# Kernel tuning notes

Hardware: AMD Instinct MI355X
Metric: run time of the kernel (lower is better)

Reference implementation:

```python
import jax, jax.numpy as jnp
import numpy as np


def setup_inputs() -> dict:
    key = jax.random.key(0)
    ks = jax.random.split(key, 8)
    B = 65536
    x = jax.random.normal(ks[0], (B, 784), dtype=jnp.float32)
    conv_w = jnp.ones((3, 3), dtype=jnp.float32)  # Parameter(ones((3,3)))
    # Linear layers stored as (in, out) weight + (out,) bias
    def lin(k, fin, fout):
        kw, kb = jax.random.split(k)
        bound = 1.0 / np.sqrt(fin)
        W = jax.random.uniform(kw, (fin, fout), minval=-bound, maxval=bound, dtype=jnp.float32)
        b = jax.random.uniform(kb, (fout,), minval=-bound, maxval=bound, dtype=jnp.float32)
        return W, b
    W1, b1 = lin(ks[1], 26 * 26, 500)
    W2, b2 = lin(ks[2], 500, 200)
    W3, b3 = lin(ks[3], 200, 10)
    return {"x": x, "conv_w": conv_w, "W1": W1, "b1": b1,
            "W2": W2, "b2": b2, "W3": W3, "b3": b3}


def reference(x, conv_w, W1, b1, W2, b2, W3, b3):
    B = x.shape[0]
    img = x.reshape(B, 1, 28, 28)  # NCHW, single channel
    kern = conv_w.reshape(1, 1, 3, 3)  # OIHW
    # valid 2D cross-correlation == torch tensordot sliding-window loop
    conv = jax.lax.conv_general_dilated(
        img, kern, window_strides=(1, 1), padding='VALID',
        dimension_numbers=('NCHW', 'OIHW', 'NCHW'))  # (B,1,26,26)
    h = conv.reshape(B, 26 * 26)
    h = jax.nn.relu(h @ W1 + b1)
    h = jax.nn.relu(h @ W2 + b2)
    return h @ W3 + b3  # (B, 10) logits
```

## Files before the change

### kernel.cpp

```cpp
#include <hip/hip_runtime.h>
#include <hip/hip_bf16.h>
#include <stdint.h>

typedef __bf16 bf16x8 __attribute__((ext_vector_type(8)));
typedef float  f32x4  __attribute__((ext_vector_type(4)));


#define KT1 25
#define NF1 32
#define KT2 16
#define NF2 16
#define KT3 8

__global__ void prep_w1(const float* __restrict__ W1, const float* __restrict__ cw,
                        __bf16* __restrict__ w1s) {
  int gid  = blockIdx.x * 256 + threadIdx.x;
  int lane = gid & 63;
  int slot = gid >> 6;
  int t = slot >> 5;
  int f = slot & 31;
  int kbase = t * 32 + ((lane >> 4) << 3);
  int n = f * 16 + (lane & 15);
  float c[9];
#pragma unroll
  for (int i = 0; i < 9; ++i) c[i] = cw[i];
  bf16x8 v;
#pragma unroll
  for (int e = 0; e < 8; ++e) {
    int k = kbase + e;
    float acc = 0.f;
    if (k < 784 && n < 500) {
      int pi = k / 28, pj = k % 28;
#pragma unroll
      for (int dr = 0; dr < 3; ++dr) {
        int r = pi - dr;
        if (r < 0 || r >= 26) continue;
#pragma unroll
        for (int dc = 0; dc < 3; ++dc) {
          int cc = pj - dc;
          if (cc < 0 || cc >= 26) continue;
          acc += c[dr * 3 + dc] * W1[(size_t)(r * 26 + cc) * 500 + n];
        }
      }
    }
    v[e] = (__bf16)acc;
  }
  *(bf16x8*)(w1s + (size_t)(slot * 64 + lane) * 8) = v;
}

__global__ void prep_w2(const float* __restrict__ W2, __bf16* __restrict__ w2s) {
  int gid  = blockIdx.x * 256 + threadIdx.x;
  int lane = gid & 63;
  int slot = gid >> 6;
  int t = slot >> 4;
  int f = slot & 15;
  int kbase = t * 32 + ((lane >> 4) << 3);
  int n = f * 16 + (lane & 15);
  bf16x8 v;
#pragma unroll
  for (int e = 0; e < 8; ++e) {
    int k = kbase + e;
    float val = (k < 500 && n < 200) ? W2[(size_t)k * 200 + n] : 0.f;
    v[e] = (__bf16)val;
  }
  *(bf16x8*)(w2s + (size_t)(slot * 64 + lane) * 8) = v;
}

__global__ void prep_w3(const float* __restrict__ W3, __bf16* __restrict__ w3s) {
  int gid  = blockIdx.x * 256 + threadIdx.x;
  int lane = gid & 63;
  int t    = gid >> 6;
  int kbase = t * 32 + ((lane >> 4) << 3);
  int n = lane & 15;
  bf16x8 v;
#pragma unroll
  for (int e = 0; e < 8; ++e) {
    int k = kbase + e;
    float val = (k < 200 && n < 10) ? W3[(size_t)k * 10 + n] : 0.f;
    v[e] = (__bf16)val;
  }
  *(bf16x8*)(w3s + (size_t)(t * 64 + lane) * 8) = v;
}

__global__ __launch_bounds__(256, 2) void mlp_fused(
    const float* __restrict__ x,
    const __bf16* __restrict__ w1s, const __bf16* __restrict__ w2s,
    const __bf16* __restrict__ w3s,
    const float* __restrict__ b1, const float* __restrict__ b2,
    const float* __restrict__ b3,
    float* __restrict__ out)
{
  __shared__ __align__(16) char xs[64 * 128];
  __shared__ __align__(16) char h1[64 * 1024];
  __shared__ float sb1[512];
  __shared__ float sb2[256];

  const int tid  = threadIdx.x;
  const int lane = tid & 63;
  const int w    = tid >> 6;
  const int lrow = lane & 15;
  const int lgrp = lane >> 4;
  const int brow = blockIdx.x * 64;

  sb1[tid]       = (tid < 500) ? b1[tid] : 0.f;
  sb1[tid + 256] = (tid + 256 < 500) ? b1[tid + 256] : 0.f;
  sb2[tid]       = (tid < 200) ? b2[tid] : 0.f;

  const f32x4 FZ = {0.f, 0.f, 0.f, 0.f};

  f32x4 acc1[4][8];
#pragma unroll
  for (int m = 0; m < 4; ++m)
#pragma unroll
    for (int f = 0; f < 8; ++f) acc1[m][f] = FZ;

  const bf16x8* w1p = (const bf16x8*)w1s + ((size_t)(w * 8) * 64 + lane);

  auto stage = [&](int t) {
#pragma unroll
    for (int i = 0; i < 2; ++i) {
      int c = i * 256 + tid;
      int r = c >> 3, q = c & 7;
      int gk = t * 32 + ((q ^ (r & 7)) << 2);
      if (gk > 780) gk = 768;
      const float* gsrc = x + (size_t)(brow + r) * 784 + gk;
      __builtin_amdgcn_global_load_lds(
          (const __attribute__((address_space(1))) void*)gsrc,
          (__attribute__((address_space(3))) void*)(xs + (size_t)(i * 256 + w * 64) * 16),
          16, 0, 0);
    }
  };

  bf16x8 bfr[8];
  stage(0);
#pragma unroll
  for (int f = 0; f < 8; ++f) bfr[f] = w1p[(size_t)f * 64];
  __syncthreads();

  for (int t = 0; t < KT1; ++t) {
    f32x4 u[4][2];
#pragma unroll
    for (int m = 0; m < 4; ++m) {
      int r  = m * 16 + lrow;
      int sw = (r & 7) << 4;
      int b  = r * 128 + ((lgrp * 32) ^ sw);
      int b2_ = r * 128 + ((lgrp * 32 + 16) ^ sw);
      u[m][0] = *(const f32x4*)(xs + b);
      u[m][1] = *(const f32x4*)(xs + b2_);
    }
    bf16x8 afr[4];
#pragma unroll
    for (int m = 0; m < 4; ++m) {
      bf16x8 a;
#pragma unroll
      for (int e = 0; e < 4; ++e) { a[e] = (__bf16)u[m][0][e]; a[e + 4] = (__bf16)u[m][1][e]; }
      afr[m] = a;
    }

#pragma unroll
    for (int f = 0; f < 4; ++f)
#pragma unroll
      for (int m = 0; m < 4; ++m)
        acc1[m][f] = __builtin_amdgcn_mfma_f32_16x16x32_bf16(afr[m], bfr[f], acc1[m][f], 0, 0, 0);

    __syncthreads();
    if (t + 1 < KT1) stage(t + 1);
#pragma unroll
    for (int f = 0; f < 4; ++f)
      bfr[f] = w1p[(size_t)((t + 1) * NF1 + f) * 64];

#pragma unroll
    for (int f = 4; f < 8; ++f)
#pragma unroll
      for (int m = 0; m < 4; ++m)
        acc1[m][f] = __builtin_amdgcn_mfma_f32_16x16x32_bf16(afr[m], bfr[f], acc1[m][f], 0, 0, 0);
#pragma unroll
    for (int f = 4; f < 8; ++f)
      bfr[f] = w1p[(size_t)((t + 1) * NF1 + f) * 64];

    __syncthreads();
  }

#pragma unroll
  for (int m = 0; m < 4; ++m) {
#pragma unroll
    for (int f = 0; f < 8; ++f) {
      int col = w * 128 + f * 16 + lrow;
      float bias = sb1[col];
#pragma unroll
      for (int r = 0; r < 4; ++r) {
        int row = m * 16 + lgrp * 4 + r;
        float v = fmaxf(acc1[m][f][r] + bias, 0.f);
        int off = row * 1024 + ((col * 2) ^ ((row & 7) << 4));
        *(__bf16*)(h1 + off) = (__bf16)v;
      }
    }
  }
  __syncthreads();

  f32x4 acc2[4][4];
#pragma unroll
  for (int m = 0; m < 4; ++m)
#pragma unroll
    for (int f = 0; f < 4; ++f) acc2[m][f] = FZ;

  const bf16x8* w2p = (const bf16x8*)w2s + ((size_t)(w * 4) * 64 + lane);

  bf16x8 b2a[4], b2b[4];
#pragma unroll
  for (int f = 0; f < 4; ++f) b2a[f] = w2p[(size_t)f * 64];

  for (int t = 0; t < KT2; t += 2) {
#pragma unroll
    for (int f = 0; f < 4; ++f) b2b[f] = w2p[(size_t)((t + 1) * NF2 + f) * 64];
    {
      bf16x8 a2[4];
#pragma unroll
      for (int m = 0; m < 4; ++m) {
        int row = m * 16 + lrow;
        int off = row * 1024 + ((t * 64 + lgrp * 16) ^ ((row & 7) << 4));
        a2[m] = *(const bf16x8*)(h1 + off);
      }
#pragma unroll
      for (int f = 0; f < 4; ++f)
#pragma unroll
        for (int m = 0; m < 4; ++m)
          acc2[m][f] = __builtin_amdgcn_mfma_f32_16x16x32_bf16(a2[m], b2a[f], acc2[m][f], 0, 0, 0);
    }
#pragma unroll
    for (int f = 0; f < 4; ++f) b2a[f] = w2p[(size_t)((t + 2) * NF2 + f) * 64];
    {
      bf16x8 a2[4];
#pragma unroll
      for (int m = 0; m < 4; ++m) {
        int row = m * 16 + lrow;
        int off = row * 1024 + (((t + 1) * 64 + lgrp * 16) ^ ((row & 7) << 4));
        a2[m] = *(const bf16x8*)(h1 + off);
      }
#pragma unroll
      for (int f = 0; f < 4; ++f)
#pragma unroll
        for (int m = 0; m < 4; ++m)
          acc2[m][f] = __builtin_amdgcn_mfma_f32_16x16x32_bf16(a2[m], b2b[f], acc2[m][f], 0, 0, 0);
    }
  }

  __syncthreads();

#pragma unroll
  for (int m = 0; m < 4; ++m) {
#pragma unroll
    for (int f = 0; f < 4; ++f) {
      int col = w * 64 + f * 16 + lrow;
      float bias = sb2[col];
#pragma unroll
      for (int r = 0; r < 4; ++r) {
        int row = m * 16 + lgrp * 4 + r;
        float v = fmaxf(acc2[m][f][r] + bias, 0.f);
        int off = row * 512 + ((col * 2) ^ ((row & 7) << 4));
        *(__bf16*)(h1 + off) = (__bf16)v;
      }
    }
  }
  __syncthreads();

  {
    f32x4 a3 = FZ;
    const bf16x8* w3p = (const bf16x8*)w3s + lane;
#pragma unroll
    for (int t = 0; t < KT3; ++t) {
      int row = w * 16 + lrow;
      int off = row * 512 + ((t * 64 + lgrp * 16) ^ ((row & 7) << 4));
      bf16x8 a = *(const bf16x8*)(h1 + off);
      a3 = __builtin_amdgcn_mfma_f32_16x16x32_bf16(a, w3p[(size_t)t * 64], a3, 0, 0, 0);
    }
    if (lrow < 10) {
      float bias = b3[lrow];
#pragma unroll
      for (int r = 0; r < 4; ++r)
        out[(size_t)(brow + w * 16 + lgrp * 4 + r) * 10 + lrow] = a3[r] + bias;
    }
  }
}

extern "C" void kernel_launch(void* const* d_in, const int* in_sizes, int n_in,
                              void* d_out, int out_size, void* d_ws, size_t ws_size,
                              hipStream_t stream) {
  const float* x  = (const float*)d_in[0];
  const float* cw = (const float*)d_in[1];
  const float* W1 = (const float*)d_in[2];
  const float* b1 = (const float*)d_in[3];
  const float* W2 = (const float*)d_in[4];
  const float* b2 = (const float*)d_in[5];
  const float* W3 = (const float*)d_in[6];
  const float* b3 = (const float*)d_in[7];
  float* out = (float*)d_out;

  __bf16* w1s = (__bf16*)d_ws;
  __bf16* w2s = w1s + (size_t)KT1 * NF1 * 64 * 8;
  __bf16* w3s = w2s + (size_t)KT2 * NF2 * 64 * 8;

  prep_w1<<<200, 256, 0, stream>>>(W1, cw, w1s);
  prep_w2<<<64, 256, 0, stream>>>(W2, w2s);
  prep_w3<<<2, 256, 0, stream>>>(W3, w3s);

  mlp_fused<<<65536 / 64, 256, 0, stream>>>(x, w1s, w2s, w3s, b1, b2, b3, out);
}
```

Before: 102.6 us.

## Triple-buffer layer-1 input staging in aliased LDS with one barrier per step

The layer-1 K loop now keeps three x-tile buffers in a single shared LDS region that is reused later for the hidden activations. Each step prefetches the tile two iterations ahead, double-buffers the W1 fragments in registers, and synchronises once through a manual vmcnt wait plus barrier instead of two __syncthreads. The loop is unrolled six ways so the buffer rotation is static. Aliasing the x buffers with h1 shrinks total LDS, which may help occupancy. The gain is deeper latency hiding, at the cost of more registers and hand-written waitcnt code that could be fragile.

```diff
diff --git a/kernel.cpp b/kernel.cpp
--- a/kernel.cpp
+++ b/kernel.cpp
@@ -90,8 +90,7 @@
     const float* __restrict__ b3,
     float* __restrict__ out)
 {
-  __shared__ __align__(16) char xs[64 * 128];
-  __shared__ __align__(16) char h1[64 * 1024];
+  __shared__ __align__(16) char smem[64 * 1024];
   __shared__ float sb1[512];
   __shared__ float sb2[256];
 
@@ -116,70 +115,94 @@
 
   const bf16x8* w1p = (const bf16x8*)w1s + ((size_t)(w * 8) * 64 + lane);
 
-  auto stage = [&](int t) {
+  auto stage_to = [&](int t, int sbo) {
+    int tt = (t > 24) ? 24 : t;
 #pragma unroll
     for (int i = 0; i < 2; ++i) {
       int c = i * 256 + tid;
       int r = c >> 3, q = c & 7;
-      int gk = t * 32 + ((q ^ (r & 7)) << 2);
+      int gk = tt * 32 + ((q ^ (r & 7)) << 2);
       if (gk > 780) gk = 768;
       const float* gsrc = x + (size_t)(brow + r) * 784 + gk;
       __builtin_amdgcn_global_load_lds(
           (const __attribute__((address_space(1))) void*)gsrc,
-          (__attribute__((address_space(3))) void*)(xs + (size_t)(i * 256 + w * 64) * 16),
+          (__attribute__((address_space(3))) void*)(smem + sbo + (size_t)(i * 256 + w * 64) * 16),
           16, 0, 0);
     }
   };
 
-  bf16x8 bfr[8];
-  stage(0);
-#pragma unroll
-  for (int f = 0; f < 8; ++f) bfr[f] = w1p[(size_t)f * 64];
-  __syncthreads();
-
-  for (int t = 0; t < KT1; ++t) {
-    f32x4 u[4][2];
+  bf16x8 bA[8], bB[8];
+
+  auto body1 = [&](int t, bf16x8 (&bc)[8], bf16x8 (&bn)[8], int rb, int sbo) {
+#pragma unroll
+    for (int f = 0; f < 8; ++f) bn[f] = w1p[(size_t)((t + 1) * NF1 + f) * 64];
+    stage_to(t + 2, sbo);
+
+    const char* xb = smem + rb;
+    f32x4 u0[4], u1[4];
 #pragma unroll
     for (int m = 0; m < 4; ++m) {
-      int r  = m * 16 + lrow;
-      int sw = (r & 7) << 4;
-      int b  = r * 128 + ((lgrp * 32) ^ sw);
-      int b2_ = r * 128 + ((lgrp * 32 + 16) ^ sw);
-      u[m][0] = *(const f32x4*)(xs + b);
-      u[m][1] = *(const f32x4*)(xs + b2_);
+      int r = m * 16 + lrow;
+      int swz = (r & 7) << 4;
+      u0[m] = *(const f32x4*)(xb + r * 128 + ((lgrp * 32) ^ swz));
+      u1[m] = *(const f32x4*)(xb + r * 128 + ((lgrp * 32 + 16) ^ swz));
     }
     bf16x8 afr[4];
 #pragma unroll
     for (int m = 0; m < 4; ++m) {
       bf16x8 a;
 #pragma unroll
-      for (int e = 0; e < 4; ++e) { a[e] = (__bf16)u[m][0][e]; a[e + 4] = (__bf16)u[m][1][e]; }
+      for (int e = 0; e < 4; ++e) { a[e] = (__bf16)u0[m][e]; a[e + 4] = (__bf16)u1[m][e]; }
       afr[m] = a;
     }
-
-#pragma unroll
-    for (int f = 0; f < 4; ++f)
+#pragma unroll
+    for (int f = 0; f < 8; ++f)
 #pragma unroll
       for (int m = 0; m < 4; ++m)
-        acc1[m][f] = __builtin_amdgcn_mfma_f32_16x16x32_bf16(afr[m], bfr[f], acc1[m][f], 0, 0, 0);
-
-    __syncthreads();
-    if (t + 1 < KT1) stage(t + 1);
-#pragma unroll
-    for (int f = 0; f < 4; ++f)
-      bfr[f] = w1p[(size_t)((t + 1) * NF1 + f) * 64];
-
-#pragma unroll
-    for (int f = 4; f < 8; ++f)
+        acc1[m][f] = __builtin_amdgcn_mfma_f32_16x16x32_bf16(afr[m], bc[f], acc1[m][f], 0, 0, 0);
+
+    asm volatile("s_waitcnt vmcnt(2)\n\ts_barrier" ::: "memory");
+  };
+
+#pragma unroll
+  for (int f = 0; f < 8; ++f) bA[f] = w1p[(size_t)f * 64];
+  stage_to(0, 0);
+  stage_to(1, 8192);
+  asm volatile("s_waitcnt vmcnt(2) lgkmcnt(0)\n\ts_barrier" ::: "memory");
+
+  for (int t = 0; t < 24; t += 6) {
+    body1(t + 0, bA, bB, 0,     16384);
+    body1(t + 1, bB, bA, 8192,  0);
+    body1(t + 2, bA, bB, 16384, 8192);
+    body1(t + 3, bB, bA, 0,     16384);
+    body1(t + 4, bA, bB, 8192,  0);
+    body1(t + 5, bB, bA, 16384, 8192);
+  }
+  {
+    const char* xb = smem;
+    f32x4 u0[4], u1[4];
+#pragma unroll
+    for (int m = 0; m < 4; ++m) {
+      int r = m * 16 + lrow;
+      int swz = (r & 7) << 4;
+      u0[m] = *(const f32x4*)(xb + r * 128 + ((lgrp * 32) ^ swz));
+      u1[m] = *(const f32x4*)(xb + r * 128 + ((lgrp * 32 + 16) ^ swz));
+    }
+    bf16x8 afr[4];
+#pragma unroll
+    for (int m = 0; m < 4; ++m) {
+      bf16x8 a;
+#pragma unroll
+      for (int e = 0; e < 4; ++e) { a[e] = (__bf16)u0[m][e]; a[e + 4] = (__bf16)u1[m][e]; }
+      afr[m] = a;
+    }
+#pragma unroll
+    for (int f = 0; f < 8; ++f)
 #pragma unroll
       for (int m = 0; m < 4; ++m)
-        acc1[m][f] = __builtin_amdgcn_mfma_f32_16x16x32_bf16(afr[m], bfr[f], acc1[m][f], 0, 0, 0);
-#pragma unroll
-    for (int f = 4; f < 8; ++f)
-      bfr[f] = w1p[(size_t)((t + 1) * NF1 + f) * 64];
-
-    __syncthreads();
-  }
+        acc1[m][f] = __builtin_amdgcn_mfma_f32_16x16x32_bf16(afr[m], bA[f], acc1[m][f], 0, 0, 0);
+  }
+  asm volatile("s_waitcnt vmcnt(0)\n\ts_barrier" ::: "memory");
 
 #pragma unroll
   for (int m = 0; m < 4; ++m) {
@@ -192,7 +215,7 @@
         int row = m * 16 + lgrp * 4 + r;
         float v = fmaxf(acc1[m][f][r] + bias, 0.f);
         int off = row * 1024 + ((col * 2) ^ ((row & 7) << 4));
-        *(__bf16*)(h1 + off) = (__bf16)v;
+        *(__bf16*)(smem + off) = (__bf16)v;
       }
     }
   }
@@ -219,7 +242,7 @@
       for (int m = 0; m < 4; ++m) {
         int row = m * 16 + lrow;
         int off = row * 1024 + ((t * 64 + lgrp * 16) ^ ((row & 7) << 4));
-        a2[m] = *(const bf16x8*)(h1 + off);
+        a2[m] = *(const bf16x8*)(smem + off);
       }
 #pragma unroll
       for (int f = 0; f < 4; ++f)
@@ -235,7 +258,7 @@
       for (int m = 0; m < 4; ++m) {
         int row = m * 16 + lrow;
         int off = row * 1024 + (((t + 1) * 64 + lgrp * 16) ^ ((row & 7) << 4));
-        a2[m] = *(const bf16x8*)(h1 + off);
+        a2[m] = *(const bf16x8*)(smem + off);
       }
 #pragma unroll
       for (int f = 0; f < 4; ++f)
@@ -258,7 +281,7 @@
         int row = m * 16 + lgrp * 4 + r;
         float v = fmaxf(acc2[m][f][r] + bias, 0.f);
         int off = row * 512 + ((col * 2) ^ ((row & 7) << 4));
-        *(__bf16*)(h1 + off) = (__bf16)v;
+        *(__bf16*)(smem + off) = (__bf16)v;
       }
     }
   }
@@ -271,7 +294,7 @@
     for (int t = 0; t < KT3; ++t) {
       int row = w * 16 + lrow;
       int off = row * 512 + ((t * 64 + lgrp * 16) ^ ((row & 7) << 4));
-      bf16x8 a = *(const bf16x8*)(h1 + off);
+      bf16x8 a = *(const bf16x8*)(smem + off);
       a3 = __builtin_amdgcn_mfma_f32_16x16x32_bf16(a, w3p[(size_t)t * 64], a3, 0, 0, 0);
     }
     if (lrow < 10) {
```

New measurement: 107.8 us. 5.0% more time.

## Double-buffer layer-1 input via registers with bf16 LDS staging and setprio

Applied to the files above, without the earlier changes.

Layer 1 no longer uses direct global-to-LDS fp32 loads. x tiles now go through registers two steps ahead, are converted to bf16 once, and are written into a double-buffered 4KB LDS tile. This replaces two __syncthreads per K-step with one barrier and removes the per-step fp32-to-bf16 conversion on the read path. It also adds s_setprio around the MFMA blocks in layers 1 and 2 to favour the matrix issue. In exchange it uses more registers for the prefetched data and the doubled weight fragments, and the handwritten waitcnt/barrier is fragile.

```diff
diff --git a/kernel.cpp b/kernel.cpp
--- a/kernel.cpp
+++ b/kernel.cpp
@@ -90,7 +90,7 @@
     const float* __restrict__ b3,
     float* __restrict__ out)
 {
-  __shared__ __align__(16) char xs[64 * 128];
+  __shared__ __align__(16) char xsm[2 * 4096];
   __shared__ __align__(16) char h1[64 * 1024];
   __shared__ float sb1[512];
   __shared__ float sb2[256];
@@ -101,6 +101,8 @@
   const int lrow = lane & 15;
   const int lgrp = lane >> 4;
   const int brow = blockIdx.x * 64;
+  const int xr   = tid >> 2;
+  const int xq   = tid & 3;
 
   sb1[tid]       = (tid < 500) ? b1[tid] : 0.f;
   sb1[tid + 256] = (tid + 256 < 500) ? b1[tid + 256] : 0.f;
@@ -114,71 +116,77 @@
 #pragma unroll
     for (int f = 0; f < 8; ++f) acc1[m][f] = FZ;
 
-  const bf16x8* w1p = (const bf16x8*)w1s + ((size_t)(w * 8) * 64 + lane);
-
-  auto stage = [&](int t) {
-#pragma unroll
-    for (int i = 0; i < 2; ++i) {
-      int c = i * 256 + tid;
-      int r = c >> 3, q = c & 7;
-      int gk = t * 32 + ((q ^ (r & 7)) << 2);
-      if (gk > 780) gk = 768;
-      const float* gsrc = x + (size_t)(brow + r) * 784 + gk;
-      __builtin_amdgcn_global_load_lds(
-          (const __attribute__((address_space(1))) void*)gsrc,
-          (__attribute__((address_space(3))) void*)(xs + (size_t)(i * 256 + w * 64) * 16),
-          16, 0, 0);
-    }
+  const bf16x8* w1p   = (const bf16x8*)w1s + ((size_t)(w * 8) * 64 + lane);
+  const float*  xbase = x + (size_t)(brow + xr) * 784;
+  const int     xswz  = (xq ^ (xr & 3)) << 4;
+  const int     xoff  = xr * 64 + xswz;
+
+  auto gload = [&](int t, f32x4 (&g)[2]) {
+    int gk = t * 32 + xq * 8;
+    if (gk > 776) gk = 776;
+    const float* p = xbase + gk;
+    g[0] = *(const f32x4*)p;
+    g[1] = *(const f32x4*)(p + 4);
   };
-
-  bf16x8 bfr[8];
-  stage(0);
-#pragma unroll
-  for (int f = 0; f < 8; ++f) bfr[f] = w1p[(size_t)f * 64];
-  __syncthreads();
-
-  for (int t = 0; t < KT1; ++t) {
-    f32x4 u[4][2];
+  auto cwrite = [&](f32x4 (&g)[2], int bw) {
+    bf16x8 v;
+#pragma unroll
+    for (int e = 0; e < 4; ++e) { v[e] = (__bf16)g[0][e]; v[e + 4] = (__bf16)g[1][e]; }
+    *(bf16x8*)(xsm + bw + xoff) = v;
+  };
+
+  f32x4  grA[2], grB[2];
+  bf16x8 bA[8], bB[8];
+
+  auto body1 = [&](int t, bf16x8 (&bc)[8], bf16x8 (&bn)[8],
+                   f32x4 (&gc)[2], f32x4 (&gl)[2], int bufR, int bufW) {
+    bf16x8 afr[4];
 #pragma unroll
     for (int m = 0; m < 4; ++m) {
-      int r  = m * 16 + lrow;
-      int sw = (r & 7) << 4;
-      int b  = r * 128 + ((lgrp * 32) ^ sw);
-      int b2_ = r * 128 + ((lgrp * 32 + 16) ^ sw);
-      u[m][0] = *(const f32x4*)(xs + b);
-      u[m][1] = *(const f32x4*)(xs + b2_);
-    }
+      int r = m * 16 + lrow;
+      afr[m] = *(const bf16x8*)(xsm + bufR + r * 64 + ((lgrp ^ (r & 3)) << 4));
+    }
+#pragma unroll
+    for (int f = 0; f < 8; ++f) bn[f] = w1p[(size_t)((t + 1) * NF1 + f) * 64];
+    gload(t + 2 > 24 ? 24 : t + 2, gl);
+    cwrite(gc, bufW);
+
+    __builtin_amdgcn_s_setprio(1);
+#pragma unroll
+    for (int f = 0; f < 8; ++f)
+#pragma unroll
+      for (int m = 0; m < 4; ++m)
+        acc1[m][f] = __builtin_amdgcn_mfma_f32_16x16x32_bf16(afr[m], bc[f], acc1[m][f], 0, 0, 0);
+    __builtin_amdgcn_s_setprio(0);
+
+    asm volatile("s_waitcnt lgkmcnt(0)\n\ts_barrier" ::: "memory");
+  };
+
+  gload(0, grA);
+#pragma unroll
+  for (int f = 0; f < 8; ++f) bA[f] = w1p[(size_t)f * 64];
+  gload(1, grB);
+  cwrite(grA, 0);
+  asm volatile("s_waitcnt lgkmcnt(0)\n\ts_barrier" ::: "memory");
+
+  for (int t = 0; t < 24; t += 2) {
+    body1(t,     bA, bB, grB, grA, 0,    4096);
+    body1(t + 1, bB, bA, grA, grB, 4096, 0);
+  }
+  {
     bf16x8 afr[4];
 #pragma unroll
     for (int m = 0; m < 4; ++m) {
-      bf16x8 a;
-#pragma unroll
-      for (int e = 0; e < 4; ++e) { a[e] = (__bf16)u[m][0][e]; a[e + 4] = (__bf16)u[m][1][e]; }
-      afr[m] = a;
-    }
-
-#pragma unroll
-    for (int f = 0; f < 4; ++f)
+      int r = m * 16 + lrow;
+      afr[m] = *(const bf16x8*)(xsm + r * 64 + ((lgrp ^ (r & 3)) << 4));
+    }
+    __builtin_amdgcn_s_setprio(1);
+#pragma unroll
+    for (int f = 0; f < 8; ++f)
 #pragma unroll
       for (int m = 0; m < 4; ++m)
-        acc1[m][f] = __builtin_amdgcn_mfma_f32_16x16x32_bf16(afr[m], bfr[f], acc1[m][f], 0, 0, 0);
-
-    __syncthreads();
-    if (t + 1 < KT1) stage(t + 1);
-#pragma unroll
-    for (int f = 0; f < 4; ++f)
-      bfr[f] = w1p[(size_t)((t + 1) * NF1 + f) * 64];
-
-#pragma unroll
-    for (int f = 4; f < 8; ++f)
-#pragma unroll
-      for (int m = 0; m < 4; ++m)
-        acc1[m][f] = __builtin_amdgcn_mfma_f32_16x16x32_bf16(afr[m], bfr[f], acc1[m][f], 0, 0, 0);
-#pragma unroll
-    for (int f = 4; f < 8; ++f)
-      bfr[f] = w1p[(size_t)((t + 1) * NF1 + f) * 64];
-
-    __syncthreads();
+        acc1[m][f] = __builtin_amdgcn_mfma_f32_16x16x32_bf16(afr[m], bA[f], acc1[m][f], 0, 0, 0);
+    __builtin_amdgcn_s_setprio(0);
   }
 
 #pragma unroll
@@ -221,11 +229,13 @@
         int off = row * 1024 + ((t * 64 + lgrp * 16) ^ ((row & 7) << 4));
         a2[m] = *(const bf16x8*)(h1 + off);
       }
+      __builtin_amdgcn_s_setprio(1);
 #pragma unroll
       for (int f = 0; f < 4; ++f)
 #pragma unroll
         for (int m = 0; m < 4; ++m)
           acc2[m][f] = __builtin_amdgcn_mfma_f32_16x16x32_bf16(a2[m], b2a[f], acc2[m][f], 0, 0, 0);
+      __builtin_amdgcn_s_setprio(0);
     }
 #pragma unroll
     for (int f = 0; f < 4; ++f) b2a[f] = w2p[(size_t)((t + 2) * NF2 + f) * 64];
@@ -237,11 +247,13 @@
         int off = row * 1024 + (((t + 1) * 64 + lgrp * 16) ^ ((row & 7) << 4));
         a2[m] = *(const bf16x8*)(h1 + off);
       }
+      __builtin_amdgcn_s_setprio(1);
 #pragma unroll
       for (int f = 0; f < 4; ++f)
 #pragma unroll
         for (int m = 0; m < 4; ++m)
           acc2[m][f] = __builtin_amdgcn_mfma_f32_16x16x32_bf16(a2[m], b2b[f], acc2[m][f], 0, 0, 0);
+      __builtin_amdgcn_s_setprio(0);
     }
   }
 
```

After: 93.04 us. -9.4%, faster.
